# Kernel optimization log

Measured on AMD Instinct MI355X. Metric: run time of the kernel, lower is better.

Reference implementation:

```python
import jax, jax.numpy as jnp
import numpy as np

L, H, HD, D, FF, V, S_LEN = 12, 12, 64, 768, 3072, 50257, 1024
NEG = jnp.finfo(jnp.float32).min


def _ln(x, g, b, eps=1e-5):
    mu = x.mean(-1, keepdims=True)
    var = ((x - mu) ** 2).mean(-1, keepdims=True)
    return (x - mu) * jax.lax.rsqrt(var + eps) * g + b


def setup_inputs() -> dict:
    key = jax.random.key(0)
    ks = jax.random.split(key, 14)
    n = lambda k, shp, s=0.02: jax.random.normal(k, shp, jnp.float32) * s
    return {
        "input_ids": jax.random.randint(ks[0], (1, S_LEN), 0, V, dtype=jnp.int32),
        "attention_mask": jnp.ones((1, S_LEN), jnp.int32),
        "wte": n(ks[1], (V, D)),
        "wpe": n(ks[2], (S_LEN, D)),
        "ln1_g": 1.0 + n(ks[3], (L, D), 0.01),
        "ln1_b": n(ks[4], (L, D), 0.01),
        "W_qkv": n(ks[5], (L, D, 3 * D)),
        "b_qkv": n(ks[6], (L, 3 * D)),
        "W_o": n(ks[7], (L, D, D)),
        "b_o": n(ks[8], (L, D)),
        "ln2_g": 1.0 + n(ks[9], (L, D), 0.01),
        "ln2_b": n(ks[10], (L, D), 0.01),
        "W_fc": n(ks[11], (L, D, FF)),
        "b_fc": n(ks[12], (L, FF)),
        "W_proj": n(ks[13], (L, FF, D)),
        "b_proj": jnp.zeros((L, D), jnp.float32),
        "S": 20, "Sa1": 21, "S2": 600,
    }


def reference(input_ids, attention_mask, wte, wpe, ln1_g, ln1_b, W_qkv, b_qkv,
              W_o, b_o, ln2_g, ln2_b, W_fc, b_fc, W_proj, b_proj, S, Sa1, S2):
    T = input_ids.shape[-1]
    h0 = wte[input_ids[0]] + wpe[:T]                      # [T, D]
    causal = jnp.tril(jnp.ones((T, T), bool))
    add_mask = (1.0 - attention_mask[0].astype(jnp.float32)) * NEG  # [T]
    scale = 1.0 / np.sqrt(HD).astype(np.float32)

    def step(h, p):
        (l1g, l1b, Wqkv, bqkv, Wo, bo, l2g, l2b, Wfc, bfc, Wp, bp) = p
        xl = _ln(h, l1g, l1b)                             # pre-block LN, [T, D]
        # ---- standard GPT-2 block forward (advances hidden state) ----
        qkv = xl @ Wqkv + bqkv
        q, k, v = jnp.split(qkv, 3, axis=-1)
        q = q.reshape(T, H, HD).transpose(1, 0, 2)        # [H, T, HD]
        k = k.reshape(T, H, HD).transpose(1, 0, 2)
        v = v.reshape(T, H, HD).transpose(1, 0, 2)
        sc = jnp.einsum('hqd,hkd->hqk', q, k) * scale
        sc = jnp.where(causal, sc, NEG) + add_mask
        ctx = jnp.einsum('hqk,hkd->hqd', jax.nn.softmax(sc, axis=-1), v)
        attn_out = ctx.transpose(1, 0, 2).reshape(T, D) @ Wo + bo
        h2 = h + attn_out
        h_new = h2 + (jax.nn.gelu(_ln(h2, l2g, l2b) @ Wfc + bfc,
                                  approximate=True) @ Wp + bp)
        # ---- manual QK circuit decomposition (pre-block hidden state) ----
        Wq, Wk, _ = jnp.split(Wqkv, 3, axis=1)            # [D, D] each
        bq, bk, _ = jnp.split(bqkv, 3, axis=0)            # [D] each
        Wmhq = Wq.reshape(D, H, HD).transpose(1, 0, 2)    # [H, D, HD]
        Wmhk = Wk.reshape(D, H, HD).transpose(1, 0, 2)
        bqh = bq.reshape(H, HD)                           # [H, HD]
        bkh = bk.reshape(H, HD)
        qc = jnp.einsum('td,hdk->htk', xl, Wmhq)          # x W_q per head
        kc = jnp.einsum('td,hdk->htk', xl, Wmhk)          # x W_k per head
        term1 = jnp.einsum('hqk,htk->hqt', qc, kc)                 # x Wq Wk^T x^T
        term2 = jnp.einsum('hk,htk->ht', bqh, kc)[:, None, :]      # bq Wk^T x^T
        term3 = jnp.einsum('hqk,hk->hq', qc, bkh)[:, :, None]      # x Wq bk^T
        term4 = jnp.einsum('hk,hk->h', bqh, bkh)[:, None, None]    # bq bk^T
        scores = (term1 + term2 + term3 + term4) * scale
        aw = jax.nn.softmax(jnp.where(causal, scores, NEG), axis=-1)  # [H, T, T]
        dup = aw[:, S2, S]
        ind = aw[:, S2, Sa1]
        prev = aw[:, -1, S2]
        return h_new, (dup, ind, prev, prev)

    params = (ln1_g, ln1_b, W_qkv, b_qkv, W_o, b_o,
              ln2_g, ln2_b, W_fc, b_fc, W_proj, b_proj)
    _, (dup, ind, prev, name) = jax.lax.scan(step, h0, params)
    return dup, ind, prev, name   # each [L, H] = [12, 12]
```

## Files before the change

### kernel.cpp

```cpp
#include <hip/hip_runtime.h>
#include <hip/hip_bf16.h>
#include <math.h>

namespace {

constexpr int T = 1024;
constexpr int D = 768;
constexpr int FF = 3072;
constexpr int H = 12;
constexpr int HD = 64;
constexpr int L = 12;
constexpr float SCALE = 0.125f;

typedef __attribute__((ext_vector_type(8))) short short8;
typedef __attribute__((ext_vector_type(4))) float floatx4;

__device__ inline unsigned short f2bf(float f) {
    __hip_bfloat16 h = __float2bfloat16(f);
    return *reinterpret_cast<unsigned short*>(&h);
}

__global__ void embed_kernel(const int* __restrict__ ids,
                             const float* __restrict__ wte,
                             const float* __restrict__ wpe,
                             float* __restrict__ h) {
    int i = blockIdx.x * blockDim.x + threadIdx.x;
    if (i >= T * D) return;
    int t = i / D, d = i % D;
    h[i] = wte[(long)ids[t] * D + d] + wpe[i];
}

__global__ __launch_bounds__(256)
void ln_kernel(const float* __restrict__ x, const float* __restrict__ g,
               const float* __restrict__ b, unsigned short* __restrict__ out) {
    int row = blockIdx.x, tid = threadIdx.x;
    const float* xr = x + (long)row * D;
    float v0 = xr[tid], v1 = xr[tid + 256], v2 = xr[tid + 512];
    __shared__ float red[4];
    __shared__ float share;
    float s = v0 + v1 + v2;
#pragma unroll
    for (int o = 32; o; o >>= 1) s += __shfl_down(s, o, 64);
    if ((tid & 63) == 0) red[tid >> 6] = s;
    __syncthreads();
    if (tid == 0) share = (red[0] + red[1] + red[2] + red[3]) * (1.0f / D);
    __syncthreads();
    float mu = share;
    float d0 = v0 - mu, d1 = v1 - mu, d2 = v2 - mu;
    float q = d0 * d0 + d1 * d1 + d2 * d2;
#pragma unroll
    for (int o = 32; o; o >>= 1) q += __shfl_down(q, o, 64);
    __syncthreads();
    if ((tid & 63) == 0) red[tid >> 6] = q;
    __syncthreads();
    if (tid == 0) share = rsqrtf((red[0] + red[1] + red[2] + red[3]) * (1.0f / D) + 1e-5f);
    __syncthreads();
    float rs = share;
    unsigned short* orow = out + (long)row * D;
    orow[tid]       = f2bf(d0 * rs * g[tid]       + b[tid]);
    orow[tid + 256] = f2bf(d1 * rs * g[tid + 256] + b[tid + 256]);
    orow[tid + 512] = f2bf(d2 * rs * g[tid + 512] + b[tid + 512]);
}

__global__ __launch_bounds__(256)
void wconvert_b(const float* __restrict__ W, unsigned short* __restrict__ WT,
                int K, int N) {
    const int zl = blockIdx.z;
    W  += (long)zl * K * N;
    WT += (long)zl * N * K;
    __shared__ float t[32][33];
    const int n0 = blockIdx.x * 32, k0 = blockIdx.y * 32;
    const int tx = threadIdx.x, ty = threadIdx.y;
#pragma unroll
    for (int i = 0; i < 4; i++)
        t[ty * 4 + i][tx] = W[(long)(k0 + ty * 4 + i) * N + n0 + tx];
    __syncthreads();
#pragma unroll
    for (int i = 0; i < 4; i++)
        WT[(long)(n0 + ty * 4 + i) * K + k0 + tx] = f2bf(t[tx][ty * 4 + i]);
}

#define GEMM_CORE(KLEN)                                                                 \
    floatx4 acc[2][2] = {};                                                             \
    {                                                                                   \
        *(short8*)&As[0][blk16][sl][0] = *(const short8*)(Ap);                          \
        *(short8*)&Bs[0][blk16][sl][0] = *(const short8*)(Bp);                          \
    }                                                                                   \
    __syncthreads();                                                                    \
    const int nsteps = (KLEN) >> 5;                                                     \
    for (int s = 0; s < nsteps; s++) {                                                  \
        const int buf = s & 1;                                                          \
        short8 nav, nbv;                                                                \
        const bool has_next = (s + 1 < nsteps);                                         \
        if (has_next) {                                                                 \
            nav = *(const short8*)(Ap + (s + 1) * 32);                                  \
            nbv = *(const short8*)(Bp + (s + 1) * 32);                                  \
        }                                                                               \
        short8 af[2], bfr[2];                                                           \
        _Pragma("unroll")                                                               \
        for (int mi = 0; mi < 2; mi++)                                                  \
            af[mi] = *(const short8*)&As[buf][(w & 1) * 2 + mi][lane][0];               \
        _Pragma("unroll")                                                               \
        for (int ni = 0; ni < 2; ni++)                                                  \
            bfr[ni] = *(const short8*)&Bs[buf][(w >> 1) * 2 + ni][lane][0];             \
        _Pragma("unroll")                                                               \
        for (int mi = 0; mi < 2; mi++)                                                  \
            _Pragma("unroll")                                                           \
            for (int ni = 0; ni < 2; ni++)                                              \
                acc[mi][ni] = __builtin_amdgcn_mfma_f32_16x16x32_bf16(                  \
                    af[mi], bfr[ni], acc[mi][ni], 0, 0, 0);                             \
        if (has_next) {                                                                 \
            const int nb = buf ^ 1;                                                     \
            *(short8*)&As[nb][blk16][sl][0] = nav;                                      \
            *(short8*)&Bs[nb][blk16][sl][0] = nbv;                                      \
        }                                                                               \
        __syncthreads();                                                                \
    }

__global__ __launch_bounds__(256)
void gemm_fused(const unsigned short* __restrict__ A, const unsigned short* __restrict__ BT,
                const float* __restrict__ bias, float* __restrict__ C,
                unsigned short* __restrict__ Cb,
                int N, int K, int flags) {
    const int row0 = blockIdx.y * 64, col0 = blockIdx.x * 64;
    const int tid = threadIdx.x;
    const int w = tid >> 6, lane = tid & 63;
    const int blk16 = tid >> 6;
    const int sl = tid & 63;
    __shared__ unsigned short As[2][4][64][8];
    __shared__ unsigned short Bs[2][4][64][8];
    const unsigned short* Ap = A + (long)(row0 + blk16 * 16 + (sl & 15)) * K + (sl >> 4) * 8;
    const unsigned short* Bp = BT + (long)(col0 + blk16 * 16 + (sl & 15)) * K + (sl >> 4) * 8;

    GEMM_CORE(K)

#pragma unroll
    for (int mi = 0; mi < 2; mi++) {
        int rg = row0 + ((w & 1) * 2 + mi) * 16 + (lane >> 4) * 4;
#pragma unroll
        for (int ni = 0; ni < 2; ni++) {
            int cg = col0 + ((w >> 1) * 2 + ni) * 16 + (lane & 15);
            float bv = (flags & 1) ? bias[cg] : 0.f;
            float bscale = ((flags & 16) && cg < D) ? SCALE : 1.0f;
#pragma unroll
            for (int r = 0; r < 4; r++) {
                float v = acc[mi][ni][r] + bv;
                if (flags & 4) {
                    float zz = 0.7978845608028654f * (v + 0.044715f * v * v * v);
                    v = v / (1.0f + __expf(-2.0f * zz));
                }
                if (flags & 8) C[(long)(rg + r) * N + cg] = v;
                Cb[(long)(rg + r) * N + cg] = f2bf(v * bscale);
            }
        }
    }
}

__global__ __launch_bounds__(256)
void gemm_bf16(const unsigned short* __restrict__ A, const unsigned short* __restrict__ BT,
               float* __restrict__ part, int N, int K, int splitK) {
    const int z = blockIdx.z;
    const int Kc = K / splitK;
    const int kb = z * Kc;
    const int row0 = blockIdx.y * 64, col0 = blockIdx.x * 64;
    const int tid = threadIdx.x;
    const int w = tid >> 6, lane = tid & 63;
    const int blk16 = tid >> 6;
    const int sl = tid & 63;
    __shared__ unsigned short As[2][4][64][8];
    __shared__ unsigned short Bs[2][4][64][8];
    const unsigned short* Ap = A + (long)(row0 + blk16 * 16 + (sl & 15)) * K + kb + (sl >> 4) * 8;
    const unsigned short* Bp = BT + (long)(col0 + blk16 * 16 + (sl & 15)) * K + kb + (sl >> 4) * 8;

    GEMM_CORE(Kc)

    float* dst = part + (long)z * T * N;
#pragma unroll
    for (int mi = 0; mi < 2; mi++) {
        int rg = row0 + ((w & 1) * 2 + mi) * 16 + (lane >> 4) * 4;
#pragma unroll
        for (int ni = 0; ni < 2; ni++) {
            int cg = col0 + ((w >> 1) * 2 + ni) * 16 + (lane & 15);
#pragma unroll
            for (int r = 0; r < 4; r++)
                dst[(long)(rg + r) * N + cg] = acc[mi][ni][r];
        }
    }
}

__global__ __launch_bounds__(256)
void reduce_ln(const float* __restrict__ part, const float* __restrict__ bias,
               const float* __restrict__ resid,
               const float* __restrict__ g, const float* __restrict__ b,
               float* __restrict__ Cres, unsigned short* __restrict__ Cln,
               int splitK) {
    const int row = blockIdx.x, tid = threadIdx.x;
    const int c0 = tid, c1 = tid + 256, c2 = tid + 512;
    const long rb = (long)row * D;
    float v0 = bias[c0] + resid[rb + c0];
    float v1 = bias[c1] + resid[rb + c1];
    float v2 = bias[c2] + resid[rb + c2];
    for (int z = 0; z < splitK; z++) {
        const float* p = part + (long)z * T * D + rb;
        v0 += p[c0]; v1 += p[c1]; v2 += p[c2];
    }
    float* crow = Cres + rb;
    crow[c0] = v0; crow[c1] = v1; crow[c2] = v2;
    __shared__ float red[4];
    __shared__ float share;
    float s = v0 + v1 + v2;
#pragma unroll
    for (int o = 32; o; o >>= 1) s += __shfl_down(s, o, 64);
    if ((tid & 63) == 0) red[tid >> 6] = s;
    __syncthreads();
    if (tid == 0) share = (red[0] + red[1] + red[2] + red[3]) * (1.0f / D);
    __syncthreads();
    float mu = share;
    float d0 = v0 - mu, d1 = v1 - mu, d2 = v2 - mu;
    float q = d0 * d0 + d1 * d1 + d2 * d2;
#pragma unroll
    for (int o = 32; o; o >>= 1) q += __shfl_down(q, o, 64);
    __syncthreads();
    if ((tid & 63) == 0) red[tid >> 6] = q;
    __syncthreads();
    if (tid == 0) share = rsqrtf((red[0] + red[1] + red[2] + red[3]) * (1.0f / D) + 1e-5f);
    __syncthreads();
    float rs = share;
    unsigned short* orow = Cln + rb;
    orow[c0] = f2bf(d0 * rs * g[c0] + b[c0]);
    orow[c1] = f2bf(d1 * rs * g[c1] + b[c1]);
    orow[c2] = f2bf(d2 * rs * g[c2] + b[c2]);
}

__global__ __launch_bounds__(256)
void flash_mfma(const unsigned short* __restrict__ qkvb, unsigned short* __restrict__ ctxb) {
    const int h = blockIdx.y;
    const int q0 = blockIdx.x * 64;
    const int tid = threadIdx.x;
    const int w = tid >> 6;
    const int l = tid & 63;
    const int lm = l & 15;
    const int g = l >> 4;

    __shared__ unsigned short Kl[64][72];
    __shared__ unsigned short Vt[64][80];
    __shared__ unsigned short Pl[4][16][72];

    short8 qf[2];
    {
        const unsigned short* qp = qkvb + (long)(q0 + w * 16 + lm) * (3 * D) + h * HD + g * 8;
        qf[0] = *(const short8*)(qp);
        qf[1] = *(const short8*)(qp + 32);
    }

    const int d8 = (tid & 7) * 8;
    const int kp = (tid >> 3) * 2;

    float m = -INFINITY, lsum = 0.f;
    floatx4 o[4] = {};
    const int qw = q0 + w * 16;
    const int nt = blockIdx.x + 1;

    for (int t = 0; t < nt; t++) {
        const int c0 = t * 64;
        __syncthreads();
        {
            const unsigned short* kr0 = qkvb + (long)(c0 + kp) * (3 * D) + D + h * HD + d8;
            const unsigned short* kr1 = kr0 + 3 * D;
            *(short8*)&Kl[kp][d8]     = *(const short8*)kr0;
            *(short8*)&Kl[kp + 1][d8] = *(const short8*)kr1;
            short8 va = *(const short8*)(kr0 + D);
            short8 vb = *(const short8*)(kr1 + D);
#pragma unroll
            for (int j = 0; j < 8; j++) {
                unsigned int pk = (unsigned)(unsigned short)va[j] |
                                  ((unsigned)(unsigned short)vb[j] << 16);
                *(unsigned int*)&Vt[d8 + j][kp] = pk;
            }
        }
        __syncthreads();

        if (c0 > qw + 15) continue;

        floatx4 st[4] = {};
#pragma unroll
        for (int ks = 0; ks < 2; ks++)
#pragma unroll
            for (int mt = 0; mt < 4; mt++) {
                short8 af = *(const short8*)&Kl[mt * 16 + lm][ks * 32 + g * 8];
                st[mt] = __builtin_amdgcn_mfma_f32_16x16x32_bf16(af, qf[ks], st[mt], 0, 0, 0);
            }

        const int qg = qw + lm;
        if (c0 + 63 > qw) {
#pragma unroll
            for (int mt = 0; mt < 4; mt++)
#pragma unroll
                for (int r = 0; r < 4; r++)
                    if (c0 + mt * 16 + g * 4 + r > qg) st[mt][r] = -INFINITY;
        }
        float tmax = -INFINITY;
#pragma unroll
        for (int mt = 0; mt < 4; mt++)
#pragma unroll
            for (int r = 0; r < 4; r++) tmax = fmaxf(tmax, st[mt][r]);
        tmax = fmaxf(tmax, __shfl_xor(tmax, 16));
        tmax = fmaxf(tmax, __shfl_xor(tmax, 32));
        float mn = fmaxf(m, tmax);
        float alpha = __expf(m - mn);
        float psum = 0.f;
        unsigned short pb[16];
#pragma unroll
        for (int mt = 0; mt < 4; mt++)
#pragma unroll
            for (int r = 0; r < 4; r++) {
                float p = __expf(st[mt][r] - mn);
                psum += p;
                pb[mt * 4 + r] = f2bf(p);
            }
        lsum = lsum * alpha + psum;
        m = mn;
#pragma unroll
        for (int mt = 0; mt < 4; mt++) {
            unsigned int p0 = (unsigned)pb[mt * 4 + 0] | ((unsigned)pb[mt * 4 + 1] << 16);
            unsigned int p1 = (unsigned)pb[mt * 4 + 2] | ((unsigned)pb[mt * 4 + 3] << 16);
            *(unsigned int*)&Pl[w][lm][mt * 16 + g * 4]     = p0;
            *(unsigned int*)&Pl[w][lm][mt * 16 + g * 4 + 2] = p1;
        }
        float ar0 = __shfl(alpha, g * 4 + 0), ar1 = __shfl(alpha, g * 4 + 1);
        float ar2 = __shfl(alpha, g * 4 + 2), ar3 = __shfl(alpha, g * 4 + 3);
#pragma unroll
        for (int fd = 0; fd < 4; fd++) {
            o[fd][0] *= ar0; o[fd][1] *= ar1; o[fd][2] *= ar2; o[fd][3] *= ar3;
        }
#pragma unroll
        for (int ks = 0; ks < 2; ks++) {
            short8 pa = *(const short8*)&Pl[w][lm][ks * 32 + g * 8];
#pragma unroll
            for (int fd = 0; fd < 4; fd++) {
                short8 vb = *(const short8*)&Vt[fd * 16 + lm][ks * 32 + g * 8];
                o[fd] = __builtin_amdgcn_mfma_f32_16x16x32_bf16(pa, vb, o[fd], 0, 0, 0);
            }
        }
    }
    float l2 = lsum + __shfl_xor(lsum, 16);
    float l4 = l2 + __shfl_xor(l2, 32);
    float linv = 1.0f / l4;
    float lr0 = __shfl(linv, g * 4 + 0), lr1 = __shfl(linv, g * 4 + 1);
    float lr2 = __shfl(linv, g * 4 + 2), lr3 = __shfl(linv, g * 4 + 3);
#pragma unroll
    for (int fd = 0; fd < 4; fd++) {
        unsigned short* cp = ctxb + (long)(qw + g * 4) * D + h * HD + fd * 16 + lm;
        cp[0 * D] = f2bf(o[fd][0] * lr0);
        cp[1 * D] = f2bf(o[fd][1] * lr1);
        cp[2 * D] = f2bf(o[fd][2] * lr2);
        cp[3 * D] = f2bf(o[fd][3] * lr3);
    }
}

__global__ __launch_bounds__(256)
void probe_kernel(const float* __restrict__ qkv,
                  const int* __restrict__ Sp, const int* __restrict__ Sa1p,
                  const int* __restrict__ S2p,
                  float* __restrict__ out, int layer) {
    const int h = blockIdx.y;
    const int which = blockIdx.x;
    const int s = *Sp, sa1 = *Sa1p, s2 = *S2p;
    const int row = which ? (T - 1) : s2;
    const int tid = threadIdx.x;
    __shared__ float qrow[64];
    __shared__ float prob[T];
    __shared__ float red[4];
    __shared__ float bshare;
    if (tid < 64) qrow[tid] = qkv[(long)row * (3 * D) + h * HD + tid];
    __syncthreads();
    float mloc = -INFINITY;
    for (int j = tid; j <= row; j += 256) {
        const float* krow = qkv + (long)j * (3 * D) + D + h * HD;
        float acc = 0;
#pragma unroll
        for (int d = 0; d < 64; d += 4) {
            float4 kv = *(const float4*)(krow + d);
            acc += qrow[d] * kv.x + qrow[d + 1] * kv.y +
                   qrow[d + 2] * kv.z + qrow[d + 3] * kv.w;
        }
        acc *= SCALE;
        prob[j] = acc;
        mloc = fmaxf(mloc, acc);
    }
#pragma unroll
    for (int o = 32; o; o >>= 1) mloc = fmaxf(mloc, __shfl_down(mloc, o, 64));
    if ((tid & 63) == 0) red[tid >> 6] = mloc;
    __syncthreads();
    if (tid == 0) bshare = fmaxf(fmaxf(red[0], red[1]), fmaxf(red[2], red[3]));
    __syncthreads();
    float m = bshare;
    float ssum = 0;
    for (int j = tid; j <= row; j += 256) {
        float e = expf(prob[j] - m);
        prob[j] = e;
        ssum += e;
    }
#pragma unroll
    for (int o = 32; o; o >>= 1) ssum += __shfl_down(ssum, o, 64);
    __syncthreads();
    if ((tid & 63) == 0) red[tid >> 6] = ssum;
    __syncthreads();
    if (tid == 0) bshare = red[0] + red[1] + red[2] + red[3];
    __syncthreads();
    float inv = 1.0f / bshare;
    if (tid == 0) {
        if (which == 0) {
            out[0 * (L * H) + layer * H + h] = prob[s] * inv;
            out[1 * (L * H) + layer * H + h] = prob[sa1] * inv;
        } else {
            out[2 * (L * H) + layer * H + h] = prob[s2] * inv;
            out[3 * (L * H) + layer * H + h] = prob[s2] * inv;
        }
    }
}

}

extern "C" void kernel_launch(void* const* d_in, const int* in_sizes, int n_in,
                              void* d_out, int out_size, void* d_ws, size_t ws_size,
                              hipStream_t stream) {
    const int*   ids    = (const int*)  d_in[0];
    const float* wte    = (const float*)d_in[2];
    const float* wpe    = (const float*)d_in[3];
    const float* ln1_g  = (const float*)d_in[4];
    const float* ln1_b  = (const float*)d_in[5];
    const float* W_qkv  = (const float*)d_in[6];
    const float* b_qkv  = (const float*)d_in[7];
    const float* W_o    = (const float*)d_in[8];
    const float* b_o    = (const float*)d_in[9];
    const float* ln2_g  = (const float*)d_in[10];
    const float* ln2_b  = (const float*)d_in[11];
    const float* W_fc   = (const float*)d_in[12];
    const float* b_fc   = (const float*)d_in[13];
    const float* W_proj = (const float*)d_in[14];
    const float* b_proj = (const float*)d_in[15];
    const int*   Sp     = (const int*)  d_in[16];
    const int*   Sa1p   = (const int*)  d_in[17];
    const int*   S2p    = (const int*)  d_in[18];
    float* out = (float*)d_out;

    float* ws   = (float*)d_ws;
    float* h    = ws;
    float* h2   = h   + (long)T * D;
    float* qkv  = h2  + (long)T * D;
    float* part = qkv + (long)T * 3 * D;
    unsigned short* xl   = (unsigned short*)(part + 4L * T * D);
    unsigned short* qkvb = xl   + (long)T * D;
    unsigned short* ctxb = qkvb + (long)T * 3 * D;
    unsigned short* fb   = ctxb + (long)T * D;
    unsigned short* wt_qkv  = fb      + (long)T * FF;
    unsigned short* wt_o    = wt_qkv  + (long)L * 3 * D * D;
    unsigned short* wt_fc   = wt_o    + (long)L * D * D;
    unsigned short* wt_proj = wt_fc   + (long)L * D * FF;

    embed_kernel<<<(T * D + 255) / 256, 256, 0, stream>>>(ids, wte, wpe, h);
    wconvert_b<<<dim3(3 * D / 32, D / 32, L), dim3(32, 8), 0, stream>>>(W_qkv, wt_qkv, D, 3 * D);
    wconvert_b<<<dim3(D / 32, D / 32, L), dim3(32, 8), 0, stream>>>(W_o, wt_o, D, D);
    wconvert_b<<<dim3(FF / 32, D / 32, L), dim3(32, 8), 0, stream>>>(W_fc, wt_fc, D, FF);
    wconvert_b<<<dim3(D / 32, FF / 32, L), dim3(32, 8), 0, stream>>>(W_proj, wt_proj, FF, D);
    ln_kernel<<<T, 256, 0, stream>>>(h, ln1_g, ln1_b, xl);

    for (int l = 0; l < L; l++) {
        gemm_fused<<<dim3(3 * D / 64, T / 64), 256, 0, stream>>>(
            xl, wt_qkv + (long)l * 3 * D * D, b_qkv + (long)l * 3 * D,
            qkv, qkvb, 3 * D, D, 1 | 8 | 16);
        probe_kernel<<<dim3(2, H), 256, 0, stream>>>(qkv, Sp, Sa1p, S2p, out, l);

        if (l == L - 1) break;

        flash_mfma<<<dim3(T / 64, H), 256, 0, stream>>>(qkvb, ctxb);
        gemm_bf16<<<dim3(D / 64, T / 64, 4), 256, 0, stream>>>(
            ctxb, wt_o + (long)l * D * D, part, D, D, 4);
        reduce_ln<<<T, 256, 0, stream>>>(
            part, b_o + (long)l * D, h, ln2_g + l * D, ln2_b + l * D, h2, xl, 4);
        gemm_fused<<<dim3(FF / 64, T / 64), 256, 0, stream>>>(
            xl, wt_fc + (long)l * D * FF, b_fc + (long)l * FF,
            nullptr, fb, FF, D, 1 | 4);
        gemm_bf16<<<dim3(D / 64, T / 64, 4), 256, 0, stream>>>(
            fb, wt_proj + (long)l * D * FF, part, D, FF, 4);
        reduce_ln<<<T, 256, 0, stream>>>(
            part, b_proj + (long)l * D, h2, ln1_g + (l + 1) * D, ln1_b + (l + 1) * D, h, xl, 4);
    }
}
```

Before: 1.461 ms.

## Replace LDS-staged GEMMs with direct-from-global MFMA tiles and drop fp32 qkv

All GEMMs drop the double-buffered shared-memory staging and instead load bf16 fragments straight from global memory into MFMA operands. Each wave now computes a 32x64 tile and each block a 128x64 tile, which halves the grid rows and removes the syncthreads barriers. The QKV GEMM also stops writing an fp32 copy, and the probe kernel reads the bf16 qkv buffer with the scale already folded in. This saves store bandwidth but the probe scores now use bf16-rounded q/k, and A/B reuse now depends on the cache rather than on LDS.

```diff
diff --git a/kernel.cpp b/kernel.cpp
--- a/kernel.cpp
+++ b/kernel.cpp
@@ -18,6 +18,11 @@
 __device__ inline unsigned short f2bf(float f) {
     __hip_bfloat16 h = __float2bfloat16(f);
     return *reinterpret_cast<unsigned short*>(&h);
+}
+__device__ inline float bf2f(unsigned short u) {
+    union { unsigned int i; float f; } c;
+    c.i = (unsigned int)u << 16;
+    return c.f;
 }
 
 __global__ void embed_kernel(const int* __restrict__ ids,
@@ -80,66 +85,45 @@
         WT[(long)(n0 + ty * 4 + i) * K + k0 + tx] = f2bf(t[tx][ty * 4 + i]);
 }
 
-#define GEMM_CORE(KLEN)                                                                 \
-    floatx4 acc[2][2] = {};                                                             \
-    {                                                                                   \
-        *(short8*)&As[0][blk16][sl][0] = *(const short8*)(Ap);                          \
-        *(short8*)&Bs[0][blk16][sl][0] = *(const short8*)(Bp);                          \
-    }                                                                                   \
-    __syncthreads();                                                                    \
-    const int nsteps = (KLEN) >> 5;                                                     \
-    for (int s = 0; s < nsteps; s++) {                                                  \
-        const int buf = s & 1;                                                          \
-        short8 nav, nbv;                                                                \
-        const bool has_next = (s + 1 < nsteps);                                         \
-        if (has_next) {                                                                 \
-            nav = *(const short8*)(Ap + (s + 1) * 32);                                  \
-            nbv = *(const short8*)(Bp + (s + 1) * 32);                                  \
-        }                                                                               \
-        short8 af[2], bfr[2];                                                           \
-        _Pragma("unroll")                                                               \
-        for (int mi = 0; mi < 2; mi++)                                                  \
-            af[mi] = *(const short8*)&As[buf][(w & 1) * 2 + mi][lane][0];               \
-        _Pragma("unroll")                                                               \
-        for (int ni = 0; ni < 2; ni++)                                                  \
-            bfr[ni] = *(const short8*)&Bs[buf][(w >> 1) * 2 + ni][lane][0];             \
-        _Pragma("unroll")                                                               \
-        for (int mi = 0; mi < 2; mi++)                                                  \
-            _Pragma("unroll")                                                           \
-            for (int ni = 0; ni < 2; ni++)                                              \
-                acc[mi][ni] = __builtin_amdgcn_mfma_f32_16x16x32_bf16(                  \
-                    af[mi], bfr[ni], acc[mi][ni], 0, 0, 0);                             \
-        if (has_next) {                                                                 \
-            const int nb = buf ^ 1;                                                     \
-            *(short8*)&As[nb][blk16][sl][0] = nav;                                      \
-            *(short8*)&Bs[nb][blk16][sl][0] = nbv;                                      \
-        }                                                                               \
-        __syncthreads();                                                                \
-    }
-
-__global__ __launch_bounds__(256)
-void gemm_fused(const unsigned short* __restrict__ A, const unsigned short* __restrict__ BT,
-                const float* __restrict__ bias, float* __restrict__ C,
-                unsigned short* __restrict__ Cb,
-                int N, int K, int flags) {
-    const int row0 = blockIdx.y * 64, col0 = blockIdx.x * 64;
-    const int tid = threadIdx.x;
-    const int w = tid >> 6, lane = tid & 63;
-    const int blk16 = tid >> 6;
-    const int sl = tid & 63;
-    __shared__ unsigned short As[2][4][64][8];
-    __shared__ unsigned short Bs[2][4][64][8];
-    const unsigned short* Ap = A + (long)(row0 + blk16 * 16 + (sl & 15)) * K + (sl >> 4) * 8;
-    const unsigned short* Bp = BT + (long)(col0 + blk16 * 16 + (sl & 15)) * K + (sl >> 4) * 8;
-
-    GEMM_CORE(K)
-
+#define DGEMM_CORE(KB, KE)                                                              \
+    const int tid = threadIdx.x;                                                        \
+    const int w = tid >> 6, lane = tid & 63;                                            \
+    const int row0 = blockIdx.y * 128 + w * 32;                                         \
+    const int col0 = blockIdx.x * 64;                                                   \
+    const int lm = lane & 15, lk = (lane >> 4) * 8;                                     \
+    const unsigned short* Ap = A + (long)(row0 + lm) * K + lk;                          \
+    const unsigned short* Bp = BT + (long)(col0 + lm) * K + lk;                         \
+    const long S16 = 16L * K;                                                           \
+    floatx4 acc[2][4] = {};                                                             \
+    _Pragma("unroll 4")                                                                 \
+    for (int k = (KB); k < (KE); k += 32) {                                             \
+        short8 a0 = *(const short8*)(Ap + k);                                           \
+        short8 a1 = *(const short8*)(Ap + S16 + k);                                     \
+        short8 b0 = *(const short8*)(Bp + k);                                           \
+        short8 b1 = *(const short8*)(Bp + S16 + k);                                     \
+        short8 b2 = *(const short8*)(Bp + 2 * S16 + k);                                 \
+        short8 b3 = *(const short8*)(Bp + 3 * S16 + k);                                 \
+        acc[0][0] = __builtin_amdgcn_mfma_f32_16x16x32_bf16(a0, b0, acc[0][0], 0, 0, 0);\
+        acc[0][1] = __builtin_amdgcn_mfma_f32_16x16x32_bf16(a0, b1, acc[0][1], 0, 0, 0);\
+        acc[0][2] = __builtin_amdgcn_mfma_f32_16x16x32_bf16(a0, b2, acc[0][2], 0, 0, 0);\
+        acc[0][3] = __builtin_amdgcn_mfma_f32_16x16x32_bf16(a0, b3, acc[0][3], 0, 0, 0);\
+        acc[1][0] = __builtin_amdgcn_mfma_f32_16x16x32_bf16(a1, b0, acc[1][0], 0, 0, 0);\
+        acc[1][1] = __builtin_amdgcn_mfma_f32_16x16x32_bf16(a1, b1, acc[1][1], 0, 0, 0);\
+        acc[1][2] = __builtin_amdgcn_mfma_f32_16x16x32_bf16(a1, b2, acc[1][2], 0, 0, 0);\
+        acc[1][3] = __builtin_amdgcn_mfma_f32_16x16x32_bf16(a1, b3, acc[1][3], 0, 0, 0);\
+    }
+
+__global__ __launch_bounds__(256)
+void gemm_direct(const unsigned short* __restrict__ A, const unsigned short* __restrict__ BT,
+                 const float* __restrict__ bias, unsigned short* __restrict__ Cb,
+                 int N, int K, int flags) {
+    DGEMM_CORE(0, K)
 #pragma unroll
     for (int mi = 0; mi < 2; mi++) {
-        int rg = row0 + ((w & 1) * 2 + mi) * 16 + (lane >> 4) * 4;
-#pragma unroll
-        for (int ni = 0; ni < 2; ni++) {
-            int cg = col0 + ((w >> 1) * 2 + ni) * 16 + (lane & 15);
+        int rg = row0 + mi * 16 + (lane >> 4) * 4;
+#pragma unroll
+        for (int ni = 0; ni < 4; ni++) {
+            int cg = col0 + ni * 16 + lm;
             float bv = (flags & 1) ? bias[cg] : 0.f;
             float bscale = ((flags & 16) && cg < D) ? SCALE : 1.0f;
 #pragma unroll
@@ -149,7 +133,6 @@
                     float zz = 0.7978845608028654f * (v + 0.044715f * v * v * v);
                     v = v / (1.0f + __expf(-2.0f * zz));
                 }
-                if (flags & 8) C[(long)(rg + r) * N + cg] = v;
                 Cb[(long)(rg + r) * N + cg] = f2bf(v * bscale);
             }
         }
@@ -157,30 +140,18 @@
 }
 
 __global__ __launch_bounds__(256)
-void gemm_bf16(const unsigned short* __restrict__ A, const unsigned short* __restrict__ BT,
-               float* __restrict__ part, int N, int K, int splitK) {
+void gemm_direct_sk(const unsigned short* __restrict__ A, const unsigned short* __restrict__ BT,
+                    float* __restrict__ part, int N, int K, int splitK) {
     const int z = blockIdx.z;
     const int Kc = K / splitK;
-    const int kb = z * Kc;
-    const int row0 = blockIdx.y * 64, col0 = blockIdx.x * 64;
-    const int tid = threadIdx.x;
-    const int w = tid >> 6, lane = tid & 63;
-    const int blk16 = tid >> 6;
-    const int sl = tid & 63;
-    __shared__ unsigned short As[2][4][64][8];
-    __shared__ unsigned short Bs[2][4][64][8];
-    const unsigned short* Ap = A + (long)(row0 + blk16 * 16 + (sl & 15)) * K + kb + (sl >> 4) * 8;
-    const unsigned short* Bp = BT + (long)(col0 + blk16 * 16 + (sl & 15)) * K + kb + (sl >> 4) * 8;
-
-    GEMM_CORE(Kc)
-
+    DGEMM_CORE(z * Kc, z * Kc + Kc)
     float* dst = part + (long)z * T * N;
 #pragma unroll
     for (int mi = 0; mi < 2; mi++) {
-        int rg = row0 + ((w & 1) * 2 + mi) * 16 + (lane >> 4) * 4;
-#pragma unroll
-        for (int ni = 0; ni < 2; ni++) {
-            int cg = col0 + ((w >> 1) * 2 + ni) * 16 + (lane & 15);
+        int rg = row0 + mi * 16 + (lane >> 4) * 4;
+#pragma unroll
+        for (int ni = 0; ni < 4; ni++) {
+            int cg = col0 + ni * 16 + lm;
 #pragma unroll
             for (int r = 0; r < 4; r++)
                 dst[(long)(rg + r) * N + cg] = acc[mi][ni][r];
@@ -359,7 +330,7 @@
 }
 
 __global__ __launch_bounds__(256)
-void probe_kernel(const float* __restrict__ qkv,
+void probe_kernel(const unsigned short* __restrict__ qkvb,
                   const int* __restrict__ Sp, const int* __restrict__ Sa1p,
                   const int* __restrict__ S2p,
                   float* __restrict__ out, int layer) {
@@ -372,19 +343,19 @@
     __shared__ float prob[T];
     __shared__ float red[4];
     __shared__ float bshare;
-    if (tid < 64) qrow[tid] = qkv[(long)row * (3 * D) + h * HD + tid];
+    if (tid < 64) qrow[tid] = bf2f(qkvb[(long)row * (3 * D) + h * HD + tid]);
     __syncthreads();
     float mloc = -INFINITY;
     for (int j = tid; j <= row; j += 256) {
-        const float* krow = qkv + (long)j * (3 * D) + D + h * HD;
+        const unsigned short* krow = qkvb + (long)j * (3 * D) + D + h * HD;
         float acc = 0;
 #pragma unroll
-        for (int d = 0; d < 64; d += 4) {
-            float4 kv = *(const float4*)(krow + d);
-            acc += qrow[d] * kv.x + qrow[d + 1] * kv.y +
-                   qrow[d + 2] * kv.z + qrow[d + 3] * kv.w;
-        }
-        acc *= SCALE;
+        for (int d = 0; d < 64; d += 8) {
+            short8 kv = *(const short8*)(krow + d);
+#pragma unroll
+            for (int e = 0; e < 8; e++)
+                acc += qrow[d + e] * bf2f((unsigned short)kv[e]);
+        }
         prob[j] = acc;
         mloc = fmaxf(mloc, acc);
     }
@@ -448,8 +419,7 @@
     float* ws   = (float*)d_ws;
     float* h    = ws;
     float* h2   = h   + (long)T * D;
-    float* qkv  = h2  + (long)T * D;
-    float* part = qkv + (long)T * 3 * D;
+    float* part = h2  + (long)T * D;
     unsigned short* xl   = (unsigned short*)(part + 4L * T * D);
     unsigned short* qkvb = xl   + (long)T * D;
     unsigned short* ctxb = qkvb + (long)T * 3 * D;
@@ -467,22 +437,21 @@
     ln_kernel<<<T, 256, 0, stream>>>(h, ln1_g, ln1_b, xl);
 
     for (int l = 0; l < L; l++) {
-        gemm_fused<<<dim3(3 * D / 64, T / 64), 256, 0, stream>>>(
+        gemm_direct<<<dim3(3 * D / 64, T / 128), 256, 0, stream>>>(
             xl, wt_qkv + (long)l * 3 * D * D, b_qkv + (long)l * 3 * D,
-            qkv, qkvb, 3 * D, D, 1 | 8 | 16);
-        probe_kernel<<<dim3(2, H), 256, 0, stream>>>(qkv, Sp, Sa1p, S2p, out, l);
+            qkvb, 3 * D, D, 1 | 16);
+        probe_kernel<<<dim3(2, H), 256, 0, stream>>>(qkvb, Sp, Sa1p, S2p, out, l);
 
         if (l == L - 1) break;
 
         flash_mfma<<<dim3(T / 64, H), 256, 0, stream>>>(qkvb, ctxb);
-        gemm_bf16<<<dim3(D / 64, T / 64, 4), 256, 0, stream>>>(
+        gemm_direct_sk<<<dim3(D / 64, T / 128, 4), 256, 0, stream>>>(
             ctxb, wt_o + (long)l * D * D, part, D, D, 4);
         reduce_ln<<<T, 256, 0, stream>>>(
             part, b_o + (long)l * D, h, ln2_g + l * D, ln2_b + l * D, h2, xl, 4);
-        gemm_fused<<<dim3(FF / 64, T / 64), 256, 0, stream>>>(
-            xl, wt_fc + (long)l * D * FF, b_fc + (long)l * FF,
-            nullptr, fb, FF, D, 1 | 4);
-        gemm_bf16<<<dim3(D / 64, T / 64, 4), 256, 0, stream>>>(
+        gemm_direct<<<dim3(FF / 64, T / 128), 256, 0, stream>>>(
+            xl, wt_fc + (long)l * D * FF, b_fc + (long)l * FF, fb, FF, D, 1 | 4);
+        gemm_direct_sk<<<dim3(D / 64, T / 128, 4), 256, 0, stream>>>(
             fb, wt_proj + (long)l * D * FF, part, D, FF, 4);
         reduce_ln<<<T, 256, 0, stream>>>(
             part, b_proj + (long)l * D, h2, ln1_g + (l + 1) * D, ln1_b + (l + 1) * D, h, xl, 4);
```

Result: slower. 1.972 ms (+35.0%).
